# Kernel tuning notes

Measured on AMD Instinct MI355X. Metric: run time of the kernel, lower is better.

Reference implementation:

```python
import jax, jax.numpy as jnp
import numpy as np

B, N, M, H = 2, 2048, 1024, 16
DK = M // H

def setup_inputs() -> dict:
    key = jax.random.key(0)
    ks = jax.random.split(key, 10)
    s = 1.0 / np.sqrt(M)
    return {
        "x": jax.random.normal(ks[0], (B, N, M), jnp.float32),
        "mask": jax.random.uniform(ks[1], (B, 1, N, N), jnp.float32),
        "Wq": jax.random.normal(ks[2], (M, M), jnp.float32) * s,
        "bq": jax.random.normal(ks[3], (M,), jnp.float32) * 0.01,
        "Wk": jax.random.normal(ks[4], (M, M), jnp.float32) * s,
        "bk": jax.random.normal(ks[5], (M,), jnp.float32) * 0.01,
        "Wv": jax.random.normal(ks[6], (M, M), jnp.float32) * s,
        "bv": jax.random.normal(ks[7], (M,), jnp.float32) * 0.01,
        "Wo": jax.random.normal(ks[8], (M, M), jnp.float32) * s,
        "bo": jax.random.normal(ks[9], (M,), jnp.float32) * 0.01,
    }

def reference(x, mask, Wq, bq, Wk, bk, Wv, bv, Wo, bo):
    Bv, Nv, Mv = x.shape
    # linear projections, split into heads: [B, H, N, DK]
    def proj(W, b):
        return (x @ W.T + b).reshape(Bv, Nv, H, DK).transpose(0, 2, 1, 3)
    q = proj(Wq, bq)
    k = proj(Wk, bk)
    v = proj(Wv, bv)
    # scaled scores [B, H, N, N], multiplicative mask pre-softmax
    scores = jnp.einsum('bhqd,bhkd->bhqk', q, k) / jnp.sqrt(jnp.float32(DK))
    scores = scores * mask  # mask broadcasts over heads
    attn = jax.nn.softmax(scores, axis=-1)
    # dropout in eval/reference: identity
    out = jnp.einsum('bhqk,bhkd->bhqd', attn, v)  # [B, H, N, DK]
    concat = out.transpose(0, 2, 1, 3).reshape(Bv, Nv, Mv)
    return concat @ Wo.T + bo
```

## Files before the change

kernel.cpp:

```cpp
#include <hip/hip_runtime.h>
#include <hip/hip_bf16.h>
#include <math.h>


typedef __attribute__((ext_vector_type(8))) short bf16x8;
typedef __attribute__((ext_vector_type(4))) float f32x4;

typedef __attribute__((address_space(1))) void gvoid;
typedef __attribute__((address_space(3))) void lvoid;

__device__ __forceinline__ void gll16(const void* g, void* l) {
    __builtin_amdgcn_global_load_lds(
        (gvoid*)(unsigned long long)g,
        (lvoid*)(unsigned int)(unsigned long long)l,
        16, 0, 0);
}

__device__ __forceinline__ short f2b(float f) {
    union { __hip_bfloat16 h; short s; } u;
    u.h = __float2bfloat16(f);
    return u.s;
}
__device__ __forceinline__ float b2f(short s) {
    union { short s; __hip_bfloat16 h; } u;
    u.s = s;
    return __bfloat162float(u.h);
}

__device__ __forceinline__ int sw8(int r, int k8) {
    return (r << 6) + ((k8 ^ (r & 7)) << 3);
}
__device__ __forceinline__ int swe(int r, int k) {
    return (r << 6) + (((k >> 3) ^ (r & 7)) << 3) + (k & 7);
}

#define PLANE   4194304UL
#define OFF_WH  (0UL * PLANE)
#define OFF_XH  (1UL * PLANE)
#define OFF_XL  (2UL * PLANE)
#define OFF_QH  (3UL * PLANE)
#define OFF_QL  (4UL * PLANE)
#define OFF_KH  (5UL * PLANE)
#define OFF_VTH (6UL * PLANE)
#define OFF_CH  (7UL * PLANE)
#define OFF_CL  (8UL * PLANE)

__global__ __launch_bounds__(256) void split_wx(
    const float* __restrict__ Wq, const float* __restrict__ Wk,
    const float* __restrict__ Wv, const float* __restrict__ Wo,
    const float* __restrict__ x,
    unsigned short* __restrict__ wh,
    unsigned short* __restrict__ xh, unsigned short* __restrict__ xl)
{
    const int i = blockIdx.x * 256 + threadIdx.x;
    if (i < 1048576) {
        const float* src = (i < 262144) ? Wq : (i < 524288) ? Wk
                         : (i < 786432) ? Wv : Wo;
        const float sc = (i < 262144) ? 0.125f : 1.0f;
        const int local = i & 262143;
        float4 v = ((const float4*)src)[local];
        short4 h;
        h.x = f2b(v.x * sc); h.y = f2b(v.y * sc);
        h.z = f2b(v.z * sc); h.w = f2b(v.w * sc);
        ((short4*)(wh + (size_t)(i >> 18) * 1048576))[local] = h;
    } else {
        const int local = i - 1048576;
        float4 v = ((const float4*)x)[local];
        short4 h, l;
        h.x = f2b(v.x); l.x = f2b(v.x - b2f(h.x));
        h.y = f2b(v.y); l.y = f2b(v.y - b2f(h.y));
        h.z = f2b(v.z); l.z = f2b(v.z - b2f(h.z));
        h.w = f2b(v.w); l.w = f2b(v.w - b2f(h.w));
        ((short4*)xh)[local] = h;
        ((short4*)xl)[local] = l;
    }
}

__global__ __launch_bounds__(256, 3) void gemm_qkv(
    unsigned short* __restrict__ wsS,
    const float* __restrict__ bq, const float* __restrict__ bk,
    const float* __restrict__ bv)
{
    __shared__ unsigned short Ash[128 * 64], Asl[128 * 64];
    __shared__ unsigned short Bsh[128 * 64];

    const int mode = blockIdx.z;
    const unsigned short* Ah = wsS + OFF_XH;
    const unsigned short* Al = wsS + OFF_XL;
    const unsigned short* Wh = wsS + OFF_WH + (size_t)mode * 1048576;

    const int tid  = threadIdx.x;
    const int lane = tid & 63;
    const int lm   = lane & 15;
    const int quad = lane >> 4;
    const int w    = tid >> 6;
    const int wr   = w >> 1, wc = w & 1;

    const int row0 = blockIdx.y * 128;
    const int col0 = blockIdx.x * 128;

    const int srow = lane >> 3;
    const int soct = (lane & 7) ^ (srow & 7);

    f32x4 acc[4][4] = {};

    if (mode == 0) {
        for (int k0 = 0; k0 < 1024; k0 += 64) {
            if (k0) __syncthreads();
            #pragma unroll
            for (int i = 0; i < 4; ++i) {
                const int rb = w * 32 + i * 8;
                gll16(&Ah[(size_t)(row0 + rb + srow) * 1024 + k0 + soct * 8],
                      &Ash[rb * 64]);
                gll16(&Al[(size_t)(row0 + rb + srow) * 1024 + k0 + soct * 8],
                      &Asl[rb * 64]);
                gll16(&Wh[(size_t)(col0 + rb + srow) * 1024 + k0 + soct * 8],
                      &Bsh[rb * 64]);
            }
            __syncthreads();
            #pragma unroll
            for (int ks = 0; ks < 2; ++ks) {
                bf16x8 afh[4], afl[4], bfh[4];
                #pragma unroll
                for (int mi = 0; mi < 4; ++mi) {
                    afh[mi] = *(const bf16x8*)&Ash[sw8(wr * 64 + mi * 16 + lm, ks * 4 + quad)];
                    afl[mi] = *(const bf16x8*)&Asl[sw8(wr * 64 + mi * 16 + lm, ks * 4 + quad)];
                }
                #pragma unroll
                for (int ni = 0; ni < 4; ++ni)
                    bfh[ni] = *(const bf16x8*)&Bsh[sw8(wc * 64 + ni * 16 + lm, ks * 4 + quad)];
                #pragma unroll
                for (int mi = 0; mi < 4; ++mi) {
                    #pragma unroll
                    for (int ni = 0; ni < 4; ++ni) {
                        acc[mi][ni] = __builtin_amdgcn_mfma_f32_16x16x32_bf16(
                            afh[mi], bfh[ni], acc[mi][ni], 0, 0, 0);
                        acc[mi][ni] = __builtin_amdgcn_mfma_f32_16x16x32_bf16(
                            afl[mi], bfh[ni], acc[mi][ni], 0, 0, 0);
                    }
                }
            }
        }
    } else {
        for (int k0 = 0; k0 < 1024; k0 += 64) {
            if (k0) __syncthreads();
            #pragma unroll
            for (int i = 0; i < 4; ++i) {
                const int rb = w * 32 + i * 8;
                gll16(&Ah[(size_t)(row0 + rb + srow) * 1024 + k0 + soct * 8],
                      &Ash[rb * 64]);
                gll16(&Wh[(size_t)(col0 + rb + srow) * 1024 + k0 + soct * 8],
                      &Bsh[rb * 64]);
            }
            __syncthreads();
            #pragma unroll
            for (int ks = 0; ks < 2; ++ks) {
                bf16x8 afh[4], bfh[4];
                #pragma unroll
                for (int mi = 0; mi < 4; ++mi)
                    afh[mi] = *(const bf16x8*)&Ash[sw8(wr * 64 + mi * 16 + lm, ks * 4 + quad)];
                #pragma unroll
                for (int ni = 0; ni < 4; ++ni)
                    bfh[ni] = *(const bf16x8*)&Bsh[sw8(wc * 64 + ni * 16 + lm, ks * 4 + quad)];
                #pragma unroll
                for (int mi = 0; mi < 4; ++mi) {
                    #pragma unroll
                    for (int ni = 0; ni < 4; ++ni)
                        acc[mi][ni] = __builtin_amdgcn_mfma_f32_16x16x32_bf16(
                            afh[mi], bfh[ni], acc[mi][ni], 0, 0, 0);
                }
            }
        }
    }

    unsigned short* qh  = wsS + OFF_QH;
    unsigned short* ql  = wsS + OFF_QL;
    unsigned short* kh  = wsS + OFF_KH;
    unsigned short* vth = wsS + OFF_VTH;
    const float* bias = (mode == 0) ? bq : (mode == 1) ? bk : bv;
    const float bscale = (mode == 0) ? 0.125f : 1.0f;

    #pragma unroll
    for (int ni = 0; ni < 4; ++ni) {
        const int f = col0 + wc * 64 + ni * 16 + lm;
        const float bvv = bias[f] * bscale;
        const int h = f >> 6, d = f & 63;
        #pragma unroll
        for (int mi = 0; mi < 4; ++mi) {
            #pragma unroll
            for (int j = 0; j < 4; ++j) {
                const int row = row0 + wr * 64 + mi * 16 + quad * 4 + j;
                const float val = acc[mi][ni][j] + bvv;
                const int bb = row >> 11, n = row & 2047;
                const short hs = f2b(val);
                if (mode == 0) {
                    const size_t idx = ((size_t)(bb * 16 + h) * 2048 + n) * 64 + d;
                    qh[idx] = hs;
                    ql[idx] = f2b(val - b2f(hs));
                } else if (mode == 1) {
                    kh[((size_t)(bb * 16 + h) * 2048 + n) * 64 + d] = hs;
                } else {
                    vth[((size_t)(bb * 16 + h) * 64 + d) * 2048 + n] = hs;
                }
            }
        }
    }
}

__global__ __launch_bounds__(256, 3) void gemm_out(
    const unsigned short* __restrict__ Ah, const unsigned short* __restrict__ Al,
    unsigned short* __restrict__ wsS,
    const float* __restrict__ bias_p, float* __restrict__ oout)
{
    __shared__ unsigned short Ash[128 * 64], Asl[128 * 64];
    __shared__ unsigned short Bsh[128 * 64];

    const unsigned short* Wh = wsS + OFF_WH + 3UL * 1048576;

    const int tid  = threadIdx.x;
    const int lane = tid & 63;
    const int lm   = lane & 15;
    const int quad = lane >> 4;
    const int w    = tid >> 6;
    const int wr   = w >> 1, wc = w & 1;

    const int row0 = blockIdx.y * 128;
    const int col0 = blockIdx.x * 128;

    const int srow = lane >> 3;
    const int soct = (lane & 7) ^ (srow & 7);

    f32x4 acc[4][4] = {};

    for (int k0 = 0; k0 < 1024; k0 += 64) {
        if (k0) __syncthreads();
        #pragma unroll
        for (int i = 0; i < 4; ++i) {
            const int rb = w * 32 + i * 8;
            gll16(&Ah[(size_t)(row0 + rb + srow) * 1024 + k0 + soct * 8],
                  &Ash[rb * 64]);
            gll16(&Al[(size_t)(row0 + rb + srow) * 1024 + k0 + soct * 8],
                  &Asl[rb * 64]);
            gll16(&Wh[(size_t)(col0 + rb + srow) * 1024 + k0 + soct * 8],
                  &Bsh[rb * 64]);
        }
        __syncthreads();
        #pragma unroll
        for (int ks = 0; ks < 2; ++ks) {
            bf16x8 afh[4], afl[4], bfh[4];
            #pragma unroll
            for (int mi = 0; mi < 4; ++mi) {
                afh[mi] = *(const bf16x8*)&Ash[sw8(wr * 64 + mi * 16 + lm, ks * 4 + quad)];
                afl[mi] = *(const bf16x8*)&Asl[sw8(wr * 64 + mi * 16 + lm, ks * 4 + quad)];
            }
            #pragma unroll
            for (int ni = 0; ni < 4; ++ni)
                bfh[ni] = *(const bf16x8*)&Bsh[sw8(wc * 64 + ni * 16 + lm, ks * 4 + quad)];
            #pragma unroll
            for (int mi = 0; mi < 4; ++mi) {
                #pragma unroll
                for (int ni = 0; ni < 4; ++ni) {
                    acc[mi][ni] = __builtin_amdgcn_mfma_f32_16x16x32_bf16(
                        afh[mi], bfh[ni], acc[mi][ni], 0, 0, 0);
                    acc[mi][ni] = __builtin_amdgcn_mfma_f32_16x16x32_bf16(
                        afl[mi], bfh[ni], acc[mi][ni], 0, 0, 0);
                }
            }
        }
    }

    #pragma unroll
    for (int ni = 0; ni < 4; ++ni) {
        const int f = col0 + wc * 64 + ni * 16 + lm;
        const float bvv = bias_p[f];
        #pragma unroll
        for (int mi = 0; mi < 4; ++mi) {
            #pragma unroll
            for (int j = 0; j < 4; ++j) {
                const int row = row0 + wr * 64 + mi * 16 + quad * 4 + j;
                oout[(size_t)row * 1024 + f] = acc[mi][ni][j] + bvv;
            }
        }
    }
}

__global__ __launch_bounds__(256, 4) void attn_fast(
    const unsigned short* __restrict__ wsS, const float* __restrict__ mask,
    unsigned short* __restrict__ ch, unsigned short* __restrict__ cl)
{
    __shared__ unsigned short Ksh[2][64 * 64];
    __shared__ unsigned short Vth[2][64 * 64];
    __shared__ unsigned short Psh[4][16 * 64];

    const int tid  = threadIdx.x;
    const int lane = tid & 63;
    const int lm   = lane & 15;
    const int quad = lane >> 4;
    const int w    = tid >> 6;

    const int q0 = blockIdx.x * 64;
    const int h  = blockIdx.y;
    const int b  = blockIdx.z;
    const int bh = b * 16 + h;

    const unsigned short* Qhg = wsS + OFF_QH  + (size_t)bh * 2048 * 64;
    const unsigned short* Qlg = wsS + OFF_QL  + (size_t)bh * 2048 * 64;
    const unsigned short* Khg = wsS + OFF_KH  + (size_t)bh * 2048 * 64;
    const unsigned short* Vhg = wsS + OFF_VTH + (size_t)bh * 64 * 2048;
    const float* Mg = mask + (size_t)b * 2048 * 2048;

    bf16x8 qfh[2], qfl[2];
    #pragma unroll
    for (int ks = 0; ks < 2; ++ks) {
        const size_t qo = (size_t)(q0 + w * 16 + lm) * 64 + ks * 32 + quad * 8;
        qfh[ks] = *(const bf16x8*)&Qhg[qo];
        qfl[ks] = *(const bf16x8*)&Qlg[qo];
    }

    const int srow = lane >> 3;
    const int soct = (lane & 7) ^ (srow & 7);

    #pragma unroll
    for (int i = 0; i < 2; ++i) {
        const int rb = w * 16 + i * 8;
        gll16(&Khg[(size_t)(rb + srow) * 64 + soct * 8],       &Ksh[0][rb * 64]);
        gll16(&Vhg[(size_t)(rb + srow) * 2048 + soct * 8],     &Vth[0][rb * 64]);
    }

    f32x4 o[4] = {};
    float lsum[4] = {0.f, 0.f, 0.f, 0.f};
    const int qwbase = q0 + w * 16 + quad * 4;

    for (int t = 0; t < 32; ++t) {
        const int k0 = t * 64;
        const int p  = t & 1;

        __syncthreads();

        if (t < 31) {
            #pragma unroll
            for (int i = 0; i < 2; ++i) {
                const int rb = w * 16 + i * 8;
                gll16(&Khg[(size_t)(k0 + 64 + rb + srow) * 64 + soct * 8],
                      &Ksh[1 - p][rb * 64]);
                gll16(&Vhg[(size_t)(rb + srow) * 2048 + k0 + 64 + soct * 8],
                      &Vth[1 - p][rb * 64]);
            }
        }

        float mreg[4][4];
        #pragma unroll
        for (int j = 0; j < 4; ++j)
            #pragma unroll
            for (int ni = 0; ni < 4; ++ni)
                mreg[j][ni] = Mg[(size_t)(qwbase + j) * 2048 + k0 + ni * 16 + lm];

        f32x4 s[4] = {};
        #pragma unroll
        for (int ks = 0; ks < 2; ++ks) {
            #pragma unroll
            for (int ni = 0; ni < 4; ++ni) {
                bf16x8 kh = *(const bf16x8*)&Ksh[p][sw8(ni * 16 + lm, ks * 4 + quad)];
                s[ni] = __builtin_amdgcn_mfma_f32_16x16x32_bf16(qfh[ks], kh, s[ni], 0, 0, 0);
                s[ni] = __builtin_amdgcn_mfma_f32_16x16x32_bf16(qfl[ks], kh, s[ni], 0, 0, 0);
            }
        }

        #pragma unroll
        for (int j = 0; j < 4; ++j) {
            #pragma unroll
            for (int ni = 0; ni < 4; ++ni) {
                const float pv = __expf(s[ni][j] * mreg[j][ni]);
                lsum[j] += pv;
                Psh[w][swe(quad * 4 + j, ni * 16 + lm)] = f2b(pv);
            }
        }

        #pragma unroll
        for (int ks = 0; ks < 2; ++ks) {
            bf16x8 ph = *(const bf16x8*)&Psh[w][sw8(lm, ks * 4 + quad)];
            #pragma unroll
            for (int ni = 0; ni < 4; ++ni) {
                bf16x8 vh = *(const bf16x8*)&Vth[p][sw8(ni * 16 + lm, ks * 4 + quad)];
                o[ni] = __builtin_amdgcn_mfma_f32_16x16x32_bf16(ph, vh, o[ni], 0, 0, 0);
            }
        }
    }

    #pragma unroll
    for (int j = 0; j < 4; ++j) {
        float ls = lsum[j];
        ls += __shfl_xor(ls, 1);
        ls += __shfl_xor(ls, 2);
        ls += __shfl_xor(ls, 4);
        ls += __shfl_xor(ls, 8);
        const float inv = 1.0f / ls;
        const int q = qwbase + j;
        #pragma unroll
        for (int ni = 0; ni < 4; ++ni) {
            const float val = o[ni][j] * inv;
            const size_t idx = ((size_t)b * 2048 + q) * 1024 + h * 64 + ni * 16 + lm;
            const short hs = f2b(val);
            ch[idx] = hs;
            cl[idx] = f2b(val - b2f(hs));
        }
    }
}

extern "C" void kernel_launch(void* const* d_in, const int* in_sizes, int n_in,
                              void* d_out, int out_size, void* d_ws, size_t ws_size,
                              hipStream_t stream) {
    const float* x    = (const float*)d_in[0];
    const float* mask = (const float*)d_in[1];
    const float* Wq   = (const float*)d_in[2];
    const float* bq   = (const float*)d_in[3];
    const float* Wk   = (const float*)d_in[4];
    const float* bk   = (const float*)d_in[5];
    const float* Wv   = (const float*)d_in[6];
    const float* bv   = (const float*)d_in[7];
    const float* Wo   = (const float*)d_in[8];
    const float* bo   = (const float*)d_in[9];

    unsigned short* wsS = (unsigned short*)d_ws;

    split_wx<<<8192, 256, 0, stream>>>(Wq, Wk, Wv, Wo, x,
        wsS + OFF_WH, wsS + OFF_XH, wsS + OFF_XL);

    gemm_qkv<<<dim3(8, 32, 3), 256, 0, stream>>>(wsS, bq, bk, bv);

    attn_fast<<<dim3(32, 16, 2), 256, 0, stream>>>(
        wsS, mask, wsS + OFF_CH, wsS + OFF_CL);

    gemm_out<<<dim3(8, 32), 256, 0, stream>>>(
        wsS + OFF_CH, wsS + OFF_CL, wsS, bo, (float*)d_out);
}
```

Measured before the change: 269.2 us.

## Double attention query tile per block to reuse K/V tiles across 128 queries

Each attention block now handles 128 query rows instead of 64, with every wave computing two 16-row sub-tiles that share each K and V fragment read from LDS. This halves the number of K/V tile loads from global memory per query and amortizes the LDS reads over twice the MFMA work. In exchange the block count is halved to 512, register pressure roughly doubles (launch bounds lowered to 2 blocks per CU), and the P staging buffer grows.

```diff
diff --git a/kernel.cpp b/kernel.cpp
--- a/kernel.cpp
+++ b/kernel.cpp
@@ -284,13 +284,13 @@
     }
 }
 
-__global__ __launch_bounds__(256, 4) void attn_fast(
+__global__ __launch_bounds__(256, 2) void attn_fast(
     const unsigned short* __restrict__ wsS, const float* __restrict__ mask,
     unsigned short* __restrict__ ch, unsigned short* __restrict__ cl)
 {
     __shared__ unsigned short Ksh[2][64 * 64];
     __shared__ unsigned short Vth[2][64 * 64];
-    __shared__ unsigned short Psh[4][16 * 64];
+    __shared__ unsigned short Psh[4][32 * 64];
 
     const int tid  = threadIdx.x;
     const int lane = tid & 63;
@@ -298,7 +298,7 @@
     const int quad = lane >> 4;
     const int w    = tid >> 6;
 
-    const int q0 = blockIdx.x * 64;
+    const int q0 = blockIdx.x * 128;
     const int h  = blockIdx.y;
     const int b  = blockIdx.z;
     const int bh = b * 16 + h;
@@ -309,13 +309,15 @@
     const unsigned short* Vhg = wsS + OFF_VTH + (size_t)bh * 64 * 2048;
     const float* Mg = mask + (size_t)b * 2048 * 2048;
 
-    bf16x8 qfh[2], qfl[2];
+    bf16x8 qfh[2][2], qfl[2][2];
     #pragma unroll
-    for (int ks = 0; ks < 2; ++ks) {
-        const size_t qo = (size_t)(q0 + w * 16 + lm) * 64 + ks * 32 + quad * 8;
-        qfh[ks] = *(const bf16x8*)&Qhg[qo];
-        qfl[ks] = *(const bf16x8*)&Qlg[qo];
-    }
+    for (int mi = 0; mi < 2; ++mi)
+        #pragma unroll
+        for (int ks = 0; ks < 2; ++ks) {
+            const size_t qo = (size_t)(q0 + w * 32 + mi * 16 + lm) * 64 + ks * 32 + quad * 8;
+            qfh[mi][ks] = *(const bf16x8*)&Qhg[qo];
+            qfl[mi][ks] = *(const bf16x8*)&Qlg[qo];
+        }
 
     const int srow = lane >> 3;
     const int soct = (lane & 7) ^ (srow & 7);
@@ -323,13 +325,13 @@
     #pragma unroll
     for (int i = 0; i < 2; ++i) {
         const int rb = w * 16 + i * 8;
-        gll16(&Khg[(size_t)(rb + srow) * 64 + soct * 8],       &Ksh[0][rb * 64]);
-        gll16(&Vhg[(size_t)(rb + srow) * 2048 + soct * 8],     &Vth[0][rb * 64]);
-    }
-
-    f32x4 o[4] = {};
-    float lsum[4] = {0.f, 0.f, 0.f, 0.f};
-    const int qwbase = q0 + w * 16 + quad * 4;
+        gll16(&Khg[(size_t)(rb + srow) * 64 + soct * 8],   &Ksh[0][rb * 64]);
+        gll16(&Vhg[(size_t)(rb + srow) * 2048 + soct * 8], &Vth[0][rb * 64]);
+    }
+
+    f32x4 o[2][4] = {};
+    float lsum[2][4] = {};
+    const int qwbase = q0 + w * 32 + quad * 4;
 
     for (int t = 0; t < 32; ++t) {
         const int k0 = t * 64;
@@ -348,63 +350,78 @@
             }
         }
 
-        float mreg[4][4];
-        #pragma unroll
-        for (int j = 0; j < 4; ++j)
-            #pragma unroll
-            for (int ni = 0; ni < 4; ++ni)
-                mreg[j][ni] = Mg[(size_t)(qwbase + j) * 2048 + k0 + ni * 16 + lm];
-
-        f32x4 s[4] = {};
+        float mreg[2][4][4];
+        #pragma unroll
+        for (int mi = 0; mi < 2; ++mi)
+            #pragma unroll
+            for (int j = 0; j < 4; ++j)
+                #pragma unroll
+                for (int ni = 0; ni < 4; ++ni)
+                    mreg[mi][j][ni] =
+                        Mg[(size_t)(qwbase + mi * 16 + j) * 2048 + k0 + ni * 16 + lm];
+
+        f32x4 s[2][4] = {};
         #pragma unroll
         for (int ks = 0; ks < 2; ++ks) {
             #pragma unroll
             for (int ni = 0; ni < 4; ++ni) {
                 bf16x8 kh = *(const bf16x8*)&Ksh[p][sw8(ni * 16 + lm, ks * 4 + quad)];
-                s[ni] = __builtin_amdgcn_mfma_f32_16x16x32_bf16(qfh[ks], kh, s[ni], 0, 0, 0);
-                s[ni] = __builtin_amdgcn_mfma_f32_16x16x32_bf16(qfl[ks], kh, s[ni], 0, 0, 0);
-            }
-        }
-
-        #pragma unroll
-        for (int j = 0; j < 4; ++j) {
-            #pragma unroll
-            for (int ni = 0; ni < 4; ++ni) {
-                const float pv = __expf(s[ni][j] * mreg[j][ni]);
-                lsum[j] += pv;
-                Psh[w][swe(quad * 4 + j, ni * 16 + lm)] = f2b(pv);
-            }
-        }
+                #pragma unroll
+                for (int mi = 0; mi < 2; ++mi) {
+                    s[mi][ni] = __builtin_amdgcn_mfma_f32_16x16x32_bf16(qfh[mi][ks], kh, s[mi][ni], 0, 0, 0);
+                    s[mi][ni] = __builtin_amdgcn_mfma_f32_16x16x32_bf16(qfl[mi][ks], kh, s[mi][ni], 0, 0, 0);
+                }
+            }
+        }
+
+        #pragma unroll
+        for (int mi = 0; mi < 2; ++mi)
+            #pragma unroll
+            for (int j = 0; j < 4; ++j) {
+                #pragma unroll
+                for (int ni = 0; ni < 4; ++ni) {
+                    const float pv = __expf(s[mi][ni][j] * mreg[mi][j][ni]);
+                    lsum[mi][j] += pv;
+                    Psh[w][swe(mi * 16 + quad * 4 + j, ni * 16 + lm)] = f2b(pv);
+                }
+            }
 
         #pragma unroll
         for (int ks = 0; ks < 2; ++ks) {
-            bf16x8 ph = *(const bf16x8*)&Psh[w][sw8(lm, ks * 4 + quad)];
+            bf16x8 ph[2];
+            #pragma unroll
+            for (int mi = 0; mi < 2; ++mi)
+                ph[mi] = *(const bf16x8*)&Psh[w][sw8(mi * 16 + lm, ks * 4 + quad)];
             #pragma unroll
             for (int ni = 0; ni < 4; ++ni) {
                 bf16x8 vh = *(const bf16x8*)&Vth[p][sw8(ni * 16 + lm, ks * 4 + quad)];
-                o[ni] = __builtin_amdgcn_mfma_f32_16x16x32_bf16(ph, vh, o[ni], 0, 0, 0);
+                #pragma unroll
+                for (int mi = 0; mi < 2; ++mi)
+                    o[mi][ni] = __builtin_amdgcn_mfma_f32_16x16x32_bf16(ph[mi], vh, o[mi][ni], 0, 0, 0);
             }
         }
     }
 
     #pragma unroll
-    for (int j = 0; j < 4; ++j) {
-        float ls = lsum[j];
-        ls += __shfl_xor(ls, 1);
-        ls += __shfl_xor(ls, 2);
-        ls += __shfl_xor(ls, 4);
-        ls += __shfl_xor(ls, 8);
-        const float inv = 1.0f / ls;
-        const int q = qwbase + j;
-        #pragma unroll
-        for (int ni = 0; ni < 4; ++ni) {
-            const float val = o[ni][j] * inv;
-            const size_t idx = ((size_t)b * 2048 + q) * 1024 + h * 64 + ni * 16 + lm;
-            const short hs = f2b(val);
-            ch[idx] = hs;
-            cl[idx] = f2b(val - b2f(hs));
-        }
-    }
+    for (int mi = 0; mi < 2; ++mi)
+        #pragma unroll
+        for (int j = 0; j < 4; ++j) {
+            float ls = lsum[mi][j];
+            ls += __shfl_xor(ls, 1);
+            ls += __shfl_xor(ls, 2);
+            ls += __shfl_xor(ls, 4);
+            ls += __shfl_xor(ls, 8);
+            const float inv = 1.0f / ls;
+            const int q = qwbase + mi * 16 + j;
+            #pragma unroll
+            for (int ni = 0; ni < 4; ++ni) {
+                const float val = o[mi][ni][j] * inv;
+                const size_t idx = ((size_t)b * 2048 + q) * 1024 + h * 64 + ni * 16 + lm;
+                const short hs = f2b(val);
+                ch[idx] = hs;
+                cl[idx] = f2b(val - b2f(hs));
+            }
+        }
 }
 
 extern "C" void kernel_launch(void* const* d_in, const int* in_sizes, int n_in,
@@ -428,7 +445,7 @@
 
     gemm_qkv<<<dim3(8, 32, 3), 256, 0, stream>>>(wsS, bq, bk, bv);
 
-    attn_fast<<<dim3(32, 16, 2), 256, 0, stream>>>(
+    attn_fast<<<dim3(16, 16, 2), 256, 0, stream>>>(
         wsS, mask, wsS + OFF_CH, wsS + OFF_CL);
 
     gemm_out<<<dim3(8, 32), 256, 0, stream>>>(
```

Result: no change. 267.2 us (-0.7%).
